# Optimization experiments

Hardware: AMD Instinct MI355X
Metric: run time of the kernel (lower is better)

The kernel has to match this reference:

```python
import jax, jax.numpy as jnp
import numpy as np

CONTEXT_SIZE = 256  # hardcoded in source; scale = context_size**-0.5, not head_size
EMBED_DIM = 384
HEAD_SIZE = 64
BATCH = 512
SEQ = 256


def setup_inputs() -> dict:
    key = jax.random.key(0)
    ks = jax.random.split(key, 7)
    s = 1.0 / np.sqrt(EMBED_DIM)
    return {
        "x": jax.random.normal(ks[0], (BATCH, SEQ, EMBED_DIM), jnp.float32),
        "Wq": jax.random.uniform(ks[1], (EMBED_DIM, HEAD_SIZE), jnp.float32, -s, s),
        "bq": jax.random.uniform(ks[2], (HEAD_SIZE,), jnp.float32, -s, s),
        "Wk": jax.random.uniform(ks[3], (EMBED_DIM, HEAD_SIZE), jnp.float32, -s, s),
        "bk": jax.random.uniform(ks[4], (HEAD_SIZE,), jnp.float32, -s, s),
        "Wv": jax.random.uniform(ks[5], (EMBED_DIM, HEAD_SIZE), jnp.float32, -s, s),
        "bv": jax.random.uniform(ks[6], (HEAD_SIZE,), jnp.float32, -s, s),
    }


def reference(x, Wq, bq, Wk, bk, Wv, bv):
    # x: [B, T, D]
    T = x.shape[1]
    q = x @ Wq + bq          # [B, T, H]
    k = x @ Wk + bk          # [B, T, H]
    v = x @ Wv + bv          # [B, T, H]
    scale = CONTEXT_SIZE ** (-0.5)  # faithful: source scales by context_size, not head_size
    scores = jnp.einsum("bth,bsh->bts", q, k) * scale  # [B, T, T]
    causal = jnp.tril(jnp.ones((T, T), dtype=bool))
    scores = jnp.where(causal, scores, -jnp.inf)
    attn = jax.nn.softmax(scores, axis=-1)
    # dropout omitted (eval mode / deterministic reference)
    return jnp.einsum("bts,bsh->bth", attn, v)  # [B, T, H]
```

## Files before the change

### kernel.cpp

```cpp
#include <hip/hip_runtime.h>
#include <hip/hip_bf16.h>
#include <stdint.h>

#define B_ 512
#define T_ 256
#define D_ 384
#define H_ 64

typedef __attribute__((ext_vector_type(8))) short bf16x8;
typedef __attribute__((ext_vector_type(4))) float f32x4;
typedef __attribute__((ext_vector_type(16))) float f32x16;

__device__ __forceinline__ unsigned short f2bf(float f) {
  union { float f; unsigned int u; } a; a.f = f;
  unsigned int r = (a.u + 0x7FFFu + ((a.u >> 16) & 1u)) >> 16;
  return (unsigned short)r;
}

__device__ __forceinline__ unsigned int pkbf(float lo, float hi) {
  unsigned int r;
  asm("v_cvt_pk_bf16_f32 %0, %1, %2" : "=v"(r) : "v"(lo), "v"(hi));
  return r;
}

__global__ void prep_wt(const float* __restrict__ Wq, const float* __restrict__ Wk,
                        const float* __restrict__ Wv, unsigned short* __restrict__ wt) {
  int idx = blockIdx.x * 256 + threadIdx.x;
  if (idx >= 192 * 384) return;
  int n = idx / 384, k = idx - n * 384;
  int sel = n >> 6, c = n & 63;
  const float* W = (sel == 0) ? Wq : ((sel == 1) ? Wk : Wv);
  wt[idx] = f2bf(W[k * 64 + c]);
}

__global__ __launch_bounds__(512) void attn_fused(
    const float* __restrict__ x, const float* __restrict__ bq,
    const float* __restrict__ bk, const float* __restrict__ bv,
    const unsigned short* __restrict__ wt, float* __restrict__ out) {
  extern __shared__ char smem[];
  const int tid = threadIdx.x;
  const int b = blockIdx.x;
  const int wv = tid >> 6, lane = tid & 63;
  const int lo4 = lane & 15, hi4 = lane >> 4;
  const int lo5 = lane & 31, hi5 = lane >> 5;

  const float* xb = x + (size_t)b * T_ * D_;

  f32x4 acc[2][12];
#pragma unroll
  for (int rt = 0; rt < 2; ++rt)
#pragma unroll
    for (int ct = 0; ct < 12; ++ct) acc[rt][ct] = (f32x4)0.0f;

  const int row0 = 32 * wv + lo4;

  for (int half = 0; half < 2; ++half) {
#pragma unroll
    for (int i = 0; i < 9; ++i) {
      int u = tid + 512 * i;
      int n = u / 24;
      int mp = u - n * 24;
      int m = mp ^ (n & 7);
      const uint4* src = reinterpret_cast<const uint4*>(wt + n * 384 + half * 192 + 8 * m);
      *reinterpret_cast<uint4*>(smem + 16 * u) = *src;
    }
    __syncthreads();
#pragma unroll
    for (int ks6 = 0; ks6 < 6; ++ks6) {
      int ks = half * 6 + ks6;
      bf16x8 afr[2];
#pragma unroll
      for (int rt = 0; rt < 2; ++rt) {
        const float* p = xb + (row0 + 16 * rt) * D_ + 32 * ks + 8 * hi4;
        float4 f0 = *reinterpret_cast<const float4*>(p);
        float4 f1 = *reinterpret_cast<const float4*>(p + 4);
        union { bf16x8 v; unsigned int w[4]; } A;
        A.w[0] = pkbf(f0.x, f0.y); A.w[1] = pkbf(f0.z, f0.w);
        A.w[2] = pkbf(f1.x, f1.y); A.w[3] = pkbf(f1.z, f1.w);
        afr[rt] = A.v;
      }
#pragma unroll
      for (int ct = 0; ct < 12; ++ct) {
        int n = 16 * ct + lo4;
        int kbyte = (64 * ks6 + 16 * hi4) ^ ((n & 7) << 4);
        bf16x8 bw = *reinterpret_cast<const bf16x8*>(smem + n * 384 + kbyte);
        acc[0][ct] = __builtin_amdgcn_mfma_f32_16x16x32_bf16(afr[0], bw, acc[0][ct], 0, 0, 0);
        acc[1][ct] = __builtin_amdgcn_mfma_f32_16x16x32_bf16(afr[1], bw, acc[1][ct], 0, 0, 0);
      }
    }
    __syncthreads();
  }

#pragma unroll
  for (int ct = 0; ct < 12; ++ct) {
    int n = 16 * ct + lo4;
    float bias = (ct < 4) ? bq[n] : ((ct < 8) ? bk[n - 64] : bv[n - 128]);
#pragma unroll
    for (int rt = 0; rt < 2; ++rt) {
      int rowb = 32 * wv + 16 * rt + 4 * hi4;
#pragma unroll
      for (int r = 0; r < 4; ++r) {
        int row = rowb + r;
        unsigned short v = f2bf(acc[rt][ct][r] + bias);
        if (ct < 4) {
          int h = n;
          *reinterpret_cast<unsigned short*>(smem + row * 128 + ((2 * h) ^ ((row & 7) << 4))) = v;
        } else if (ct < 8) {
          int h = n - 64;
          *reinterpret_cast<unsigned short*>(smem + 32768 + row * 128 + ((2 * h) ^ ((row & 7) << 4))) = v;
        } else {
          int h = n - 128;
          *reinterpret_cast<unsigned short*>(smem + 65536 + h * 512 + ((2 * row) ^ ((h & 7) << 4))) = v;
        }
      }
    }
  }
  __syncthreads();

  const float cexp = 0.09016844005555897f;

  bf16x8 qf[4];
  {
    int row = 32 * wv + lo5;
#pragma unroll
    for (int s = 0; s < 4; ++s)
      qf[s] = *reinterpret_cast<const bf16x8*>(
          smem + row * 128 + (((32 * s + 16 * hi5)) ^ ((row & 7) << 4)));
  }

  f32x16 o0 = (f32x16)0.0f, o1 = (f32x16)0.0f;
  float lsum = 0.0f;

  for (int kb = 0; kb <= wv; ++kb) {
    f32x16 st = (f32x16)0.0f;
    {
      int row = 32 * kb + lo5;
#pragma unroll
      for (int s = 0; s < 4; ++s) {
        bf16x8 kf = *reinterpret_cast<const bf16x8*>(
            smem + 32768 + row * 128 + (((32 * s + 16 * hi5)) ^ ((row & 7) << 4)));
        st = __builtin_amdgcn_mfma_f32_32x32x16_bf16(kf, qf[s], st, 0, 0, 0);
      }
    }
    float p[16];
#pragma unroll
    for (int r = 0; r < 16; ++r) {
      float e = exp2f(cexp * st[r]);
      if (kb == wv) {
        int keyl = (r & 3) + 8 * (r >> 2) + 4 * hi5;
        if (keyl > lo5) e = 0.0f;
      }
      p[r] = e;
      lsum += e;
    }

    union { bf16x8 v; unsigned int w[4]; } A0, A1;
    {
      unsigned int X0 = pkbf(p[0], p[1]),  X1 = pkbf(p[2], p[3]);
      unsigned int Y0 = pkbf(p[4], p[5]),  Y1 = pkbf(p[6], p[7]);
      unsigned int X0p = (unsigned int)__shfl_xor((int)X0, 32);
      unsigned int X1p = (unsigned int)__shfl_xor((int)X1, 32);
      unsigned int Y0p = (unsigned int)__shfl_xor((int)Y0, 32);
      unsigned int Y1p = (unsigned int)__shfl_xor((int)Y1, 32);
      A0.w[0] = hi5 ? Y0p : X0;
      A0.w[1] = hi5 ? Y1p : X1;
      A0.w[2] = hi5 ? Y0  : X0p;
      A0.w[3] = hi5 ? Y1  : X1p;
      unsigned int Z0 = pkbf(p[8], p[9]),   Z1 = pkbf(p[10], p[11]);
      unsigned int W0 = pkbf(p[12], p[13]), W1 = pkbf(p[14], p[15]);
      unsigned int Z0p = (unsigned int)__shfl_xor((int)Z0, 32);
      unsigned int Z1p = (unsigned int)__shfl_xor((int)Z1, 32);
      unsigned int W0p = (unsigned int)__shfl_xor((int)W0, 32);
      unsigned int W1p = (unsigned int)__shfl_xor((int)W1, 32);
      A1.w[0] = hi5 ? W0p : Z0;
      A1.w[1] = hi5 ? W1p : Z1;
      A1.w[2] = hi5 ? W0  : Z0p;
      A1.w[3] = hi5 ? W1  : Z1p;
    }
#pragma unroll
    for (int s2 = 0; s2 < 2; ++s2) {
      bf16x8 pa = s2 ? A1.v : A0.v;
      int kk = 32 * kb + 16 * s2 + 8 * hi5;
#pragma unroll
      for (int ht = 0; ht < 2; ++ht) {
        int h = 32 * ht + lo5;
        bf16x8 vf = *reinterpret_cast<const bf16x8*>(
            smem + 65536 + h * 512 + (((2 * kk)) ^ ((h & 7) << 4)));
        if (ht == 0) o0 = __builtin_amdgcn_mfma_f32_32x32x16_bf16(pa, vf, o0, 0, 0, 0);
        else         o1 = __builtin_amdgcn_mfma_f32_32x32x16_bf16(pa, vf, o1, 0, 0, 0);
      }
    }
  }

  lsum += __shfl_xor(lsum, 32);
  float inv = 1.0f / lsum;
  float* ob = out + (size_t)b * T_ * H_;
#pragma unroll
  for (int r = 0; r < 16; ++r) {
    int ridx = (r & 3) + 8 * (r >> 2) + 4 * hi5;
    float invr = __shfl(inv, ridx);
    int row = 32 * wv + ridx;
    ob[row * H_ + lo5]      = o0[r] * invr;
    ob[row * H_ + 32 + lo5] = o1[r] * invr;
  }
}

extern "C" void kernel_launch(void* const* d_in, const int* in_sizes, int n_in,
                              void* d_out, int out_size, void* d_ws, size_t ws_size,
                              hipStream_t stream) {
  const float* x  = (const float*)d_in[0];
  const float* Wq = (const float*)d_in[1];
  const float* bq = (const float*)d_in[2];
  const float* Wk = (const float*)d_in[3];
  const float* bk = (const float*)d_in[4];
  const float* Wv = (const float*)d_in[5];
  const float* bv = (const float*)d_in[6];
  unsigned short* wt = (unsigned short*)d_ws;
  float* out = (float*)d_out;

  prep_wt<<<288, 256, 0, stream>>>(Wq, Wk, Wv, wt);
  attn_fused<<<B_, 512, 98304, stream>>>(x, bq, bk, bv, wt, out);
}
```

Before: 65.71 us.

## Double-buffer x and weight tiles into LDS via async global_load_lds

Replaces the QKV projection's direct global x loads and two-phase weight staging with a 12-step K loop that streams both x and the bf16 weights into double-buffered, swizzled LDS using global_load_lds. Loads for tile t+2 are issued while tile t is computed, with manual vmcnt waits and barriers. The aim is to hide global memory latency behind the MFMAs and coalesce the x reads. The cost is two barriers per tile and fragile hand-written vmcnt counts.

```diff
diff --git a/kernel.cpp b/kernel.cpp
--- a/kernel.cpp
+++ b/kernel.cpp
@@ -21,6 +21,12 @@
   unsigned int r;
   asm("v_cvt_pk_bf16_f32 %0, %1, %2" : "=v"(r) : "v"(lo), "v"(hi));
   return r;
+}
+
+__device__ __forceinline__ void gld16(const void* g, void* l) {
+  __builtin_amdgcn_global_load_lds(
+      (const __attribute__((address_space(1))) unsigned int*)g,
+      (__attribute__((address_space(3))) unsigned int*)l, 16, 0, 0);
 }
 
 __global__ void prep_wt(const float* __restrict__ Wq, const float* __restrict__ Wk,
@@ -52,43 +58,73 @@
 #pragma unroll
     for (int ct = 0; ct < 12; ++ct) acc[rt][ct] = (f32x4)0.0f;
 
-  const int row0 = 32 * wv + lo4;
-
-  for (int half = 0; half < 2; ++half) {
-#pragma unroll
-    for (int i = 0; i < 9; ++i) {
-      int u = tid + 512 * i;
-      int n = u / 24;
-      int mp = u - n * 24;
-      int m = mp ^ (n & 7);
-      const uint4* src = reinterpret_cast<const uint4*>(wt + n * 384 + half * 192 + 8 * m);
-      *reinterpret_cast<uint4*>(smem + 16 * u) = *src;
-    }
-    __syncthreads();
-#pragma unroll
-    for (int ks6 = 0; ks6 < 6; ++ks6) {
-      int ks = half * 6 + ks6;
-      bf16x8 afr[2];
-#pragma unroll
-      for (int rt = 0; rt < 2; ++rt) {
-        const float* p = xb + (row0 + 16 * rt) * D_ + 32 * ks + 8 * hi4;
-        float4 f0 = *reinterpret_cast<const float4*>(p);
-        float4 f1 = *reinterpret_cast<const float4*>(p + 4);
-        union { bf16x8 v; unsigned int w[4]; } A;
-        A.w[0] = pkbf(f0.x, f0.y); A.w[1] = pkbf(f0.z, f0.w);
-        A.w[2] = pkbf(f1.x, f1.y); A.w[3] = pkbf(f1.z, f1.w);
-        afr[rt] = A.v;
-      }
-#pragma unroll
-      for (int ct = 0; ct < 12; ++ct) {
-        int n = 16 * ct + lo4;
-        int kbyte = (64 * ks6 + 16 * hi4) ^ ((n & 7) << 4);
-        bf16x8 bw = *reinterpret_cast<const bf16x8*>(smem + n * 384 + kbyte);
-        acc[0][ct] = __builtin_amdgcn_mfma_f32_16x16x32_bf16(afr[0], bw, acc[0][ct], 0, 0, 0);
-        acc[1][ct] = __builtin_amdgcn_mfma_f32_16x16x32_bf16(afr[1], bw, acc[1][ct], 0, 0, 0);
-      }
-    }
-    __syncthreads();
+  auto issue_tile = [&](int t) {
+    char* bx = smem + (t & 1) * 32768;
+    char* bw = smem + 65536 + (t & 1) * 12288;
+#pragma unroll
+    for (int i = 0; i < 4; ++i) {
+      int ub = 256 * wv + 64 * i;
+      int u = ub + lane;
+      int row = u >> 3;
+      int c = (u & 7) ^ (row & 7);
+      gld16((const char*)xb + (size_t)row * 1536 + 128 * t + 16 * c, bx + 16 * ub);
+    }
+    if (wv < 6) {
+#pragma unroll
+      for (int i = 0; i < 2; ++i) {
+        int ub = 128 * wv + 64 * i;
+        int u = ub + lane;
+        int n = u >> 2;
+        int c = (u & 3) ^ (n & 3);
+        gld16((const char*)wt + (size_t)n * 768 + 64 * t + 16 * c, bw + 16 * ub);
+      }
+    }
+  };
+
+  auto compute_tile = [&](int t) {
+    const char* bx = smem + (t & 1) * 32768;
+    const char* bw = smem + 65536 + (t & 1) * 12288;
+    bf16x8 afr[2];
+#pragma unroll
+    for (int rt = 0; rt < 2; ++rt) {
+      int row = 32 * wv + 16 * rt + lo4;
+      int u0 = 8 * row + ((2 * hi4) ^ (row & 7));
+      int u1 = 8 * row + ((2 * hi4 + 1) ^ (row & 7));
+      float4 f0 = *reinterpret_cast<const float4*>(bx + 16 * u0);
+      float4 f1 = *reinterpret_cast<const float4*>(bx + 16 * u1);
+      union { bf16x8 v; unsigned int w[4]; } A;
+      A.w[0] = pkbf(f0.x, f0.y); A.w[1] = pkbf(f0.z, f0.w);
+      A.w[2] = pkbf(f1.x, f1.y); A.w[3] = pkbf(f1.z, f1.w);
+      afr[rt] = A.v;
+    }
+#pragma unroll
+    for (int ct = 0; ct < 12; ++ct) {
+      int n = 16 * ct + lo4;
+      int uB = 4 * n + (hi4 ^ (n & 3));
+      bf16x8 bwf = *reinterpret_cast<const bf16x8*>(bw + 16 * uB);
+      acc[0][ct] = __builtin_amdgcn_mfma_f32_16x16x32_bf16(afr[0], bwf, acc[0][ct], 0, 0, 0);
+      acc[1][ct] = __builtin_amdgcn_mfma_f32_16x16x32_bf16(afr[1], bwf, acc[1][ct], 0, 0, 0);
+    }
+  };
+
+  issue_tile(0);
+  issue_tile(1);
+#pragma unroll 1
+  for (int t = 0; t < 12; ++t) {
+    if (t < 11) {
+      if (wv < 6) asm volatile("s_waitcnt vmcnt(6)" ::: "memory");
+      else        asm volatile("s_waitcnt vmcnt(4)" ::: "memory");
+    } else {
+      asm volatile("s_waitcnt vmcnt(0)" ::: "memory");
+    }
+    __builtin_amdgcn_sched_barrier(0);
+    __builtin_amdgcn_s_barrier();
+    __builtin_amdgcn_sched_barrier(0);
+    compute_tile(t);
+    __builtin_amdgcn_sched_barrier(0);
+    __builtin_amdgcn_s_barrier();
+    __builtin_amdgcn_sched_barrier(0);
+    if (t < 10) issue_tile(t + 2);
   }
 
 #pragma unroll
```

Measured after the change: 66.07 us. Within noise of the previous version (+0.6%).

## Split fused attention into separate QKV GEMM and attention kernels

Applied to the files above, without the earlier changes.

The single fused kernel, one 512-thread block per batch with 96KB of LDS, is replaced by a QKV projection GEMM over 128-row tiles (1024 blocks of 256 threads) that writes bf16 Q, K and transposed V to workspace, followed by an attention kernel that stages K and V into LDS with global_load_lds. The split aims to raise occupancy and balance work, since in the fused kernel the causal loop left the early waves idle while the GEMM phase used heavy LDS. The cost is an extra round trip of Q, K and V through global memory and an additional kernel launch.

```diff
diff --git a/kernel.cpp b/kernel.cpp
--- a/kernel.cpp
+++ b/kernel.cpp
@@ -21,6 +21,12 @@
   unsigned int r;
   asm("v_cvt_pk_bf16_f32 %0, %1, %2" : "=v"(r) : "v"(lo), "v"(hi));
   return r;
+}
+
+__device__ __forceinline__ void gld16(const void* g, void* l) {
+  __builtin_amdgcn_global_load_lds(
+      (const __attribute__((address_space(1))) unsigned int*)g,
+      (__attribute__((address_space(3))) unsigned int*)l, 16, 0, 0);
 }
 
 __global__ void prep_wt(const float* __restrict__ Wq, const float* __restrict__ Wk,
@@ -33,112 +39,163 @@
   wt[idx] = f2bf(W[k * 64 + c]);
 }
 
-__global__ __launch_bounds__(512) void attn_fused(
+__global__ __launch_bounds__(256, 3) void qkv_gemm(
     const float* __restrict__ x, const float* __restrict__ bq,
     const float* __restrict__ bk, const float* __restrict__ bv,
-    const unsigned short* __restrict__ wt, float* __restrict__ out) {
+    const unsigned short* __restrict__ wt,
+    unsigned short* __restrict__ qg, unsigned short* __restrict__ kg,
+    unsigned short* __restrict__ vtg) {
+  extern __shared__ char smem[];
+  const int tid = threadIdx.x;
+  const int w = tid >> 6, lane = tid & 63;
+  const int lo4 = lane & 15, hi4 = lane >> 4;
+  const int bid = blockIdx.x;
+  const size_t rowbase = 128 * (size_t)bid;
+
+  f32x4 acc[2][12];
+#pragma unroll
+  for (int rt = 0; rt < 2; ++rt)
+#pragma unroll
+    for (int ct = 0; ct < 12; ++ct) acc[rt][ct] = (f32x4)0.0f;
+
+  const char* xb = (const char*)x + rowbase * 1536;
+
+  for (int qtr = 0; qtr < 4; ++qtr) {
+#pragma unroll
+    for (int i = 0; i < 12; ++i) {
+      int m = tid + 256 * i;
+      int n = m >> 4;
+      int cl = m & 15;
+      int cg = cl ^ (n & 7);
+      int csrc = (cg < 12) ? cg : (cg - 12);
+      gld16((const char*)wt + n * 768 + qtr * 192 + 16 * csrc, smem + 16 * m);
+    }
+    asm volatile("s_waitcnt vmcnt(0)" ::: "memory");
+    __syncthreads();
+#pragma unroll
+    for (int ks = 0; ks < 3; ++ks) {
+      bf16x8 afr[2];
+#pragma unroll
+      for (int rt = 0; rt < 2; ++rt) {
+        int row = 32 * w + 16 * rt + lo4;
+        const char* p = xb + (size_t)row * 1536 + 384 * qtr + 128 * ks + 32 * hi4;
+        float4 f0 = *reinterpret_cast<const float4*>(p);
+        float4 f1 = *reinterpret_cast<const float4*>(p + 16);
+        union { bf16x8 v; unsigned int u[4]; } A;
+        A.u[0] = pkbf(f0.x, f0.y); A.u[1] = pkbf(f0.z, f0.w);
+        A.u[2] = pkbf(f1.x, f1.y); A.u[3] = pkbf(f1.z, f1.w);
+        afr[rt] = A.v;
+      }
+#pragma unroll
+      for (int ct = 0; ct < 12; ++ct) {
+        int n = 16 * ct + lo4;
+        bf16x8 bw = *reinterpret_cast<const bf16x8*>(
+            smem + n * 256 + (((64 * ks + 16 * hi4)) ^ ((n & 7) << 4)));
+        acc[0][ct] = __builtin_amdgcn_mfma_f32_16x16x32_bf16(afr[0], bw, acc[0][ct], 0, 0, 0);
+        acc[1][ct] = __builtin_amdgcn_mfma_f32_16x16x32_bf16(afr[1], bw, acc[1][ct], 0, 0, 0);
+      }
+    }
+    __syncthreads();
+  }
+
+#pragma unroll
+  for (int ct = 0; ct < 12; ++ct) {
+    int n = 16 * ct + lo4;
+    float bias = (ct < 4) ? bq[n] : ((ct < 8) ? bk[n - 64] : bv[n - 128]);
+#pragma unroll
+    for (int rt = 0; rt < 2; ++rt) {
+      int rowb = 32 * w + 16 * rt + 4 * hi4;
+#pragma unroll
+      for (int r = 0; r < 4; ++r) {
+        *reinterpret_cast<unsigned short*>(smem + (rowb + r) * 400 + 2 * n) =
+            f2bf(acc[rt][ct][r] + bias);
+      }
+    }
+  }
+  __syncthreads();
+
+#pragma unroll
+  for (int it = 0; it < 13; ++it) {
+    int g = tid + 256 * it;
+    if (g < 3200) {
+      int row = g / 25;
+      int c = g - 25 * row;
+      if (c < 16) {
+        uint4 val = *reinterpret_cast<const uint4*>(smem + row * 400 + 16 * c);
+        size_t grow = rowbase + row;
+        if (c < 8)
+          *reinterpret_cast<uint4*>((char*)qg + grow * 128 + 16 * c) = val;
+        else
+          *reinterpret_cast<uint4*>((char*)kg + grow * 128 + 16 * (c - 8)) = val;
+      }
+    }
+  }
+
+  {
+    int b = bid >> 1;
+    int t0 = (bid & 1) * 128;
+#pragma unroll
+    for (int it = 0; it < 4; ++it) {
+      int task = tid + 256 * it;
+      int h = task & 63;
+      int rc = task >> 6;
+      union { unsigned short s[8]; uint4 v; } P;
+#pragma unroll
+      for (int j = 0; j < 8; ++j)
+        P.s[j] = *reinterpret_cast<const unsigned short*>(smem + (8 * rc + j) * 400 + 256 + 2 * h);
+      *reinterpret_cast<uint4*>((char*)vtg + (size_t)b * 32768 + h * 512 + (t0 + 8 * rc) * 2) = P.v;
+    }
+  }
+}
+
+__global__ __launch_bounds__(512, 4) void attn2(
+    const unsigned short* __restrict__ qg, const unsigned short* __restrict__ kg,
+    const unsigned short* __restrict__ vtg, float* __restrict__ out) {
   extern __shared__ char smem[];
   const int tid = threadIdx.x;
   const int b = blockIdx.x;
   const int wv = tid >> 6, lane = tid & 63;
-  const int lo4 = lane & 15, hi4 = lane >> 4;
   const int lo5 = lane & 31, hi5 = lane >> 5;
 
-  const float* xb = x + (size_t)b * T_ * D_;
-
-  f32x4 acc[2][12];
-#pragma unroll
-  for (int rt = 0; rt < 2; ++rt)
-#pragma unroll
-    for (int ct = 0; ct < 12; ++ct) acc[rt][ct] = (f32x4)0.0f;
-
-  const int row0 = 32 * wv + lo4;
-
-  for (int half = 0; half < 2; ++half) {
-#pragma unroll
-    for (int i = 0; i < 9; ++i) {
-      int u = tid + 512 * i;
-      int n = u / 24;
-      int mp = u - n * 24;
-      int m = mp ^ (n & 7);
-      const uint4* src = reinterpret_cast<const uint4*>(wt + n * 384 + half * 192 + 8 * m);
-      *reinterpret_cast<uint4*>(smem + 16 * u) = *src;
-    }
-    __syncthreads();
-#pragma unroll
-    for (int ks6 = 0; ks6 < 6; ++ks6) {
-      int ks = half * 6 + ks6;
-      bf16x8 afr[2];
-#pragma unroll
-      for (int rt = 0; rt < 2; ++rt) {
-        const float* p = xb + (row0 + 16 * rt) * D_ + 32 * ks + 8 * hi4;
-        float4 f0 = *reinterpret_cast<const float4*>(p);
-        float4 f1 = *reinterpret_cast<const float4*>(p + 4);
-        union { bf16x8 v; unsigned int w[4]; } A;
-        A.w[0] = pkbf(f0.x, f0.y); A.w[1] = pkbf(f0.z, f0.w);
-        A.w[2] = pkbf(f1.x, f1.y); A.w[3] = pkbf(f1.z, f1.w);
-        afr[rt] = A.v;
-      }
-#pragma unroll
-      for (int ct = 0; ct < 12; ++ct) {
-        int n = 16 * ct + lo4;
-        int kbyte = (64 * ks6 + 16 * hi4) ^ ((n & 7) << 4);
-        bf16x8 bw = *reinterpret_cast<const bf16x8*>(smem + n * 384 + kbyte);
-        acc[0][ct] = __builtin_amdgcn_mfma_f32_16x16x32_bf16(afr[0], bw, acc[0][ct], 0, 0, 0);
-        acc[1][ct] = __builtin_amdgcn_mfma_f32_16x16x32_bf16(afr[1], bw, acc[1][ct], 0, 0, 0);
-      }
-    }
-    __syncthreads();
-  }
-
-#pragma unroll
-  for (int ct = 0; ct < 12; ++ct) {
-    int n = 16 * ct + lo4;
-    float bias = (ct < 4) ? bq[n] : ((ct < 8) ? bk[n - 64] : bv[n - 128]);
-#pragma unroll
-    for (int rt = 0; rt < 2; ++rt) {
-      int rowb = 32 * wv + 16 * rt + 4 * hi4;
-#pragma unroll
-      for (int r = 0; r < 4; ++r) {
-        int row = rowb + r;
-        unsigned short v = f2bf(acc[rt][ct][r] + bias);
-        if (ct < 4) {
-          int h = n;
-          *reinterpret_cast<unsigned short*>(smem + row * 128 + ((2 * h) ^ ((row & 7) << 4))) = v;
-        } else if (ct < 8) {
-          int h = n - 64;
-          *reinterpret_cast<unsigned short*>(smem + 32768 + row * 128 + ((2 * h) ^ ((row & 7) << 4))) = v;
-        } else {
-          int h = n - 128;
-          *reinterpret_cast<unsigned short*>(smem + 65536 + h * 512 + ((2 * row) ^ ((h & 7) << 4))) = v;
-        }
-      }
-    }
-  }
-  __syncthreads();
-
-  const float cexp = 0.09016844005555897f;
+  const char* qb = (const char*)qg + (size_t)b * 32768;
+  const char* kb = (const char*)kg + (size_t)b * 32768;
+  const char* vb = (const char*)vtg + (size_t)b * 32768;
+
+#pragma unroll
+  for (int i = 0; i < 4; ++i) {
+    int m = tid + 512 * i;
+    int row = m >> 3, c = m & 7;
+    gld16(kb + row * 128 + 16 * (c ^ (row & 7)), smem + 16 * m);
+  }
+#pragma unroll
+  for (int i = 0; i < 4; ++i) {
+    int m = tid + 512 * i;
+    int h = m >> 5, c = m & 31;
+    gld16(vb + h * 512 + 16 * (c ^ (h & 7)), smem + 32768 + 16 * m);
+  }
 
   bf16x8 qf[4];
   {
     int row = 32 * wv + lo5;
 #pragma unroll
     for (int s = 0; s < 4; ++s)
-      qf[s] = *reinterpret_cast<const bf16x8*>(
-          smem + row * 128 + (((32 * s + 16 * hi5)) ^ ((row & 7) << 4)));
-  }
-
+      qf[s] = *reinterpret_cast<const bf16x8*>(qb + row * 128 + 32 * s + 16 * hi5);
+  }
+  asm volatile("s_waitcnt vmcnt(0)" ::: "memory");
+  __syncthreads();
+
+  const float cexp = 0.09016844005555897f;
   f32x16 o0 = (f32x16)0.0f, o1 = (f32x16)0.0f;
   float lsum = 0.0f;
 
-  for (int kb = 0; kb <= wv; ++kb) {
+  for (int kb2 = 0; kb2 <= wv; ++kb2) {
     f32x16 st = (f32x16)0.0f;
     {
-      int row = 32 * kb + lo5;
+      int row = 32 * kb2 + lo5;
 #pragma unroll
       for (int s = 0; s < 4; ++s) {
         bf16x8 kf = *reinterpret_cast<const bf16x8*>(
-            smem + 32768 + row * 128 + (((32 * s + 16 * hi5)) ^ ((row & 7) << 4)));
+            smem + row * 128 + (((32 * s + 16 * hi5)) ^ ((row & 7) << 4)));
         st = __builtin_amdgcn_mfma_f32_32x32x16_bf16(kf, qf[s], st, 0, 0, 0);
       }
     }
@@ -146,7 +203,7 @@
 #pragma unroll
     for (int r = 0; r < 16; ++r) {
       float e = exp2f(cexp * st[r]);
-      if (kb == wv) {
+      if (kb2 == wv) {
         int keyl = (r & 3) + 8 * (r >> 2) + 4 * hi5;
         if (keyl > lo5) e = 0.0f;
       }
@@ -180,12 +237,12 @@
 #pragma unroll
     for (int s2 = 0; s2 < 2; ++s2) {
       bf16x8 pa = s2 ? A1.v : A0.v;
-      int kk = 32 * kb + 16 * s2 + 8 * hi5;
+      int kk = 32 * kb2 + 16 * s2 + 8 * hi5;
 #pragma unroll
       for (int ht = 0; ht < 2; ++ht) {
         int h = 32 * ht + lo5;
         bf16x8 vf = *reinterpret_cast<const bf16x8*>(
-            smem + 65536 + h * 512 + (((2 * kk)) ^ ((h & 7) << 4)));
+            smem + 32768 + h * 512 + (((2 * kk)) ^ ((h & 7) << 4)));
         if (ht == 0) o0 = __builtin_amdgcn_mfma_f32_32x32x16_bf16(pa, vf, o0, 0, 0, 0);
         else         o1 = __builtin_amdgcn_mfma_f32_32x32x16_bf16(pa, vf, o1, 0, 0, 0);
       }
@@ -215,9 +272,14 @@
   const float* bk = (const float*)d_in[4];
   const float* Wv = (const float*)d_in[5];
   const float* bv = (const float*)d_in[6];
-  unsigned short* wt = (unsigned short*)d_ws;
   float* out = (float*)d_out;
 
+  unsigned short* qg  = (unsigned short*)d_ws;
+  unsigned short* kg  = (unsigned short*)((char*)d_ws + 16777216);
+  unsigned short* vtg = (unsigned short*)((char*)d_ws + 33554432);
+  unsigned short* wt  = (unsigned short*)((char*)d_ws + 50331648);
+
   prep_wt<<<288, 256, 0, stream>>>(Wq, Wk, Wv, wt);
-  attn_fused<<<B_, 512, 98304, stream>>>(x, bq, bk, bv, wt, out);
-}
+  qkv_gemm<<<1024, 256, 51200, stream>>>(x, bq, bk, bv, wt, qg, kg, vtg);
+  attn2<<<B_, 512, 65536, stream>>>(qg, kg, vtg, out);
+}
```

Result: slower. 144.8 us (+120.3%).

## Cut LDS to 64KB, stage weights via global_load_lds, prefetch x

Applied to the files above, without the earlier changes.

Shared memory drops from 96KB to 64KB. Q fragments are now loaded into registers before K overwrites Q's region, and the weight staging is split into quarters. Weights are copied with direct global-to-LDS loads, and x tiles are software-prefetched one step ahead of their MFMA use. Launch bounds ask for 4 blocks per CU, which may force register spills given the large accumulator arrays.

```diff
diff --git a/kernel.cpp b/kernel.cpp
--- a/kernel.cpp
+++ b/kernel.cpp
@@ -21,6 +21,12 @@
   unsigned int r;
   asm("v_cvt_pk_bf16_f32 %0, %1, %2" : "=v"(r) : "v"(lo), "v"(hi));
   return r;
+}
+
+__device__ __forceinline__ void gld16(const void* g, void* l) {
+  __builtin_amdgcn_global_load_lds(
+      (const __attribute__((address_space(1))) unsigned int*)g,
+      (__attribute__((address_space(3))) unsigned int*)l, 16, 0, 0);
 }
 
 __global__ void prep_wt(const float* __restrict__ Wq, const float* __restrict__ Wk,
@@ -33,7 +39,7 @@
   wt[idx] = f2bf(W[k * 64 + c]);
 }
 
-__global__ __launch_bounds__(512) void attn_fused(
+__global__ __launch_bounds__(512, 4) void attn_fused(
     const float* __restrict__ x, const float* __restrict__ bq,
     const float* __restrict__ bk, const float* __restrict__ bv,
     const unsigned short* __restrict__ wt, float* __restrict__ out) {
@@ -44,7 +50,8 @@
   const int lo4 = lane & 15, hi4 = lane >> 4;
   const int lo5 = lane & 31, hi5 = lane >> 5;
 
-  const float* xb = x + (size_t)b * T_ * D_;
+  const char* xb = (const char*)x + (size_t)b * T_ * D_ * 4;
+  const int row0 = 32 * wv + lo4;
 
   f32x4 acc[2][12];
 #pragma unroll
@@ -52,49 +59,90 @@
 #pragma unroll
     for (int ct = 0; ct < 12; ++ct) acc[rt][ct] = (f32x4)0.0f;
 
-  const int row0 = 32 * wv + lo4;
-
-  for (int half = 0; half < 2; ++half) {
-#pragma unroll
-    for (int i = 0; i < 9; ++i) {
-      int u = tid + 512 * i;
-      int n = u / 24;
-      int mp = u - n * 24;
-      int m = mp ^ (n & 7);
-      const uint4* src = reinterpret_cast<const uint4*>(wt + n * 384 + half * 192 + 8 * m);
-      *reinterpret_cast<uint4*>(smem + 16 * u) = *src;
-    }
+  auto ldx = [&](float4* dst, int ksg) {
+#pragma unroll
+    for (int rt = 0; rt < 2; ++rt) {
+      const char* p = xb + (size_t)(row0 + 16 * rt) * 1536 + 128 * ksg + 32 * hi4;
+      dst[2 * rt]     = *reinterpret_cast<const float4*>(p);
+      dst[2 * rt + 1] = *reinterpret_cast<const float4*>(p + 16);
+    }
+  };
+
+  auto step = [&](const float4* xr, int ks3) {
+    bf16x8 afr[2];
+#pragma unroll
+    for (int rt = 0; rt < 2; ++rt) {
+      union { bf16x8 v; unsigned int u[4]; } A;
+      A.u[0] = pkbf(xr[2 * rt].x, xr[2 * rt].y);
+      A.u[1] = pkbf(xr[2 * rt].z, xr[2 * rt].w);
+      A.u[2] = pkbf(xr[2 * rt + 1].x, xr[2 * rt + 1].y);
+      A.u[3] = pkbf(xr[2 * rt + 1].z, xr[2 * rt + 1].w);
+      afr[rt] = A.v;
+    }
+#pragma unroll
+    for (int ct = 0; ct < 12; ++ct) {
+      int n = 16 * ct + lo4;
+      bf16x8 bw = *reinterpret_cast<const bf16x8*>(
+          smem + n * 256 + (((64 * ks3 + 16 * hi4)) ^ ((n & 7) << 4)));
+      acc[0][ct] = __builtin_amdgcn_mfma_f32_16x16x32_bf16(afr[0], bw, acc[0][ct], 0, 0, 0);
+      acc[1][ct] = __builtin_amdgcn_mfma_f32_16x16x32_bf16(afr[1], bw, acc[1][ct], 0, 0, 0);
+    }
+  };
+
+  for (int qtr = 0; qtr < 4; ++qtr) {
+    float4 xA[4], xB[4];
+    ldx(xA, 3 * qtr + 0);
+    ldx(xB, 3 * qtr + 1);
+#pragma unroll
+    for (int i = 0; i < 6; ++i) {
+      int m = tid + 512 * i;
+      int n = m >> 4;
+      int cl = m & 15;
+      int cg = cl ^ (n & 7);
+      int csrc = (cg < 12) ? cg : (cg - 12);
+      gld16((const char*)wt + n * 768 + qtr * 192 + 16 * csrc, smem + 16 * m);
+    }
+    asm volatile("s_waitcnt vmcnt(0)" ::: "memory");
     __syncthreads();
-#pragma unroll
-    for (int ks6 = 0; ks6 < 6; ++ks6) {
-      int ks = half * 6 + ks6;
-      bf16x8 afr[2];
-#pragma unroll
-      for (int rt = 0; rt < 2; ++rt) {
-        const float* p = xb + (row0 + 16 * rt) * D_ + 32 * ks + 8 * hi4;
-        float4 f0 = *reinterpret_cast<const float4*>(p);
-        float4 f1 = *reinterpret_cast<const float4*>(p + 4);
-        union { bf16x8 v; unsigned int w[4]; } A;
-        A.w[0] = pkbf(f0.x, f0.y); A.w[1] = pkbf(f0.z, f0.w);
-        A.w[2] = pkbf(f1.x, f1.y); A.w[3] = pkbf(f1.z, f1.w);
-        afr[rt] = A.v;
-      }
-#pragma unroll
-      for (int ct = 0; ct < 12; ++ct) {
-        int n = 16 * ct + lo4;
-        int kbyte = (64 * ks6 + 16 * hi4) ^ ((n & 7) << 4);
-        bf16x8 bw = *reinterpret_cast<const bf16x8*>(smem + n * 384 + kbyte);
-        acc[0][ct] = __builtin_amdgcn_mfma_f32_16x16x32_bf16(afr[0], bw, acc[0][ct], 0, 0, 0);
-        acc[1][ct] = __builtin_amdgcn_mfma_f32_16x16x32_bf16(afr[1], bw, acc[1][ct], 0, 0, 0);
-      }
-    }
+
+    step(xA, 0);
+    ldx(xA, 3 * qtr + 2);
+    step(xB, 1);
+    step(xA, 2);
     __syncthreads();
   }
 
 #pragma unroll
-  for (int ct = 0; ct < 12; ++ct) {
+  for (int ct = 0; ct < 4; ++ct) {
     int n = 16 * ct + lo4;
-    float bias = (ct < 4) ? bq[n] : ((ct < 8) ? bk[n - 64] : bv[n - 128]);
+    float bias = bq[n];
+#pragma unroll
+    for (int rt = 0; rt < 2; ++rt) {
+      int rowb = 32 * wv + 16 * rt + 4 * hi4;
+#pragma unroll
+      for (int r = 0; r < 4; ++r) {
+        int row = rowb + r;
+        *reinterpret_cast<unsigned short*>(
+            smem + row * 128 + ((2 * n) ^ ((row & 7) << 4))) = f2bf(acc[rt][ct][r] + bias);
+      }
+    }
+  }
+  __syncthreads();
+
+  bf16x8 qf[4];
+  {
+    int row = 32 * wv + lo5;
+#pragma unroll
+    for (int s = 0; s < 4; ++s)
+      qf[s] = *reinterpret_cast<const bf16x8*>(
+          smem + row * 128 + (((32 * s + 16 * hi5)) ^ ((row & 7) << 4)));
+  }
+  __syncthreads();
+
+#pragma unroll
+  for (int ct = 4; ct < 12; ++ct) {
+    int n = 16 * ct + lo4;
+    float bias = (ct < 8) ? bk[n - 64] : bv[n - 128];
 #pragma unroll
     for (int rt = 0; rt < 2; ++rt) {
       int rowb = 32 * wv + 16 * rt + 4 * hi4;
@@ -102,15 +150,14 @@
       for (int r = 0; r < 4; ++r) {
         int row = rowb + r;
         unsigned short v = f2bf(acc[rt][ct][r] + bias);
-        if (ct < 4) {
-          int h = n;
-          *reinterpret_cast<unsigned short*>(smem + row * 128 + ((2 * h) ^ ((row & 7) << 4))) = v;
-        } else if (ct < 8) {
+        if (ct < 8) {
           int h = n - 64;
-          *reinterpret_cast<unsigned short*>(smem + 32768 + row * 128 + ((2 * h) ^ ((row & 7) << 4))) = v;
+          *reinterpret_cast<unsigned short*>(
+              smem + row * 128 + ((2 * h) ^ ((row & 7) << 4))) = v;
         } else {
           int h = n - 128;
-          *reinterpret_cast<unsigned short*>(smem + 65536 + h * 512 + ((2 * row) ^ ((h & 7) << 4))) = v;
+          *reinterpret_cast<unsigned short*>(
+              smem + 32768 + h * 512 + ((2 * row) ^ ((h & 7) << 4))) = v;
         }
       }
     }
@@ -118,27 +165,17 @@
   __syncthreads();
 
   const float cexp = 0.09016844005555897f;
-
-  bf16x8 qf[4];
-  {
-    int row = 32 * wv + lo5;
-#pragma unroll
-    for (int s = 0; s < 4; ++s)
-      qf[s] = *reinterpret_cast<const bf16x8*>(
-          smem + row * 128 + (((32 * s + 16 * hi5)) ^ ((row & 7) << 4)));
-  }
-
   f32x16 o0 = (f32x16)0.0f, o1 = (f32x16)0.0f;
   float lsum = 0.0f;
 
-  for (int kb = 0; kb <= wv; ++kb) {
+  for (int kb2 = 0; kb2 <= wv; ++kb2) {
     f32x16 st = (f32x16)0.0f;
     {
-      int row = 32 * kb + lo5;
+      int row = 32 * kb2 + lo5;
 #pragma unroll
       for (int s = 0; s < 4; ++s) {
         bf16x8 kf = *reinterpret_cast<const bf16x8*>(
-            smem + 32768 + row * 128 + (((32 * s + 16 * hi5)) ^ ((row & 7) << 4)));
+            smem + row * 128 + (((32 * s + 16 * hi5)) ^ ((row & 7) << 4)));
         st = __builtin_amdgcn_mfma_f32_32x32x16_bf16(kf, qf[s], st, 0, 0, 0);
       }
     }
@@ -146,7 +183,7 @@
 #pragma unroll
     for (int r = 0; r < 16; ++r) {
       float e = exp2f(cexp * st[r]);
-      if (kb == wv) {
+      if (kb2 == wv) {
         int keyl = (r & 3) + 8 * (r >> 2) + 4 * hi5;
         if (keyl > lo5) e = 0.0f;
       }
@@ -180,12 +217,12 @@
 #pragma unroll
     for (int s2 = 0; s2 < 2; ++s2) {
       bf16x8 pa = s2 ? A1.v : A0.v;
-      int kk = 32 * kb + 16 * s2 + 8 * hi5;
+      int kk = 32 * kb2 + 16 * s2 + 8 * hi5;
 #pragma unroll
       for (int ht = 0; ht < 2; ++ht) {
         int h = 32 * ht + lo5;
         bf16x8 vf = *reinterpret_cast<const bf16x8*>(
-            smem + 65536 + h * 512 + (((2 * kk)) ^ ((h & 7) << 4)));
+            smem + 32768 + h * 512 + (((2 * kk)) ^ ((h & 7) << 4)));
         if (ht == 0) o0 = __builtin_amdgcn_mfma_f32_32x32x16_bf16(pa, vf, o0, 0, 0, 0);
         else         o1 = __builtin_amdgcn_mfma_f32_32x32x16_bf16(pa, vf, o1, 0, 0, 0);
       }
@@ -219,5 +256,5 @@
   float* out = (float*)d_out;
 
   prep_wt<<<288, 256, 0, stream>>>(Wq, Wk, Wv, wt);
-  attn_fused<<<B_, 512, 98304, stream>>>(x, bq, bk, bv, wt, out);
-}
+  attn_fused<<<B_, 512, 65536, stream>>>(x, bq, bk, bv, wt, out);
+}
```

New measurement: 118.5 us. +80.4%, slower.
